# Kernel optimization log

Hardware: AMD Instinct MI355X
Metric: run time of the kernel (lower is better)

The kernel has to match this reference:

```python
import jax, jax.numpy as jnp
import numpy as np

N_FEAT = 1024
N_HEAD = 8
CONTEXT_SIZES = [21, 41]
HPS = N_HEAD // len(CONTEXT_SIZES)  # heads per scale = 4


def setup_inputs() -> dict:
    key = jax.random.key(0)
    ks = jax.random.split(key, 9)
    B, T, D = 4, 1024, N_FEAT
    s = 1.0 / np.sqrt(D)
    return {
        "query": jax.random.normal(ks[0], (B, T, D), dtype=jnp.float32),
        "key": jax.random.normal(ks[1], (B, T, D), dtype=jnp.float32),
        "value": jax.random.normal(ks[2], (B, T, D), dtype=jnp.float32),
        # weights stored [in, out] (torch Linear applies x @ W.T)
        "W_qv": jax.random.normal(ks[3], (D, 2 * D), dtype=jnp.float32) * s,
        "W2_0": jax.random.normal(ks[4], (D, HPS * CONTEXT_SIZES[0]), dtype=jnp.float32) * s,
        "W2_1": jax.random.normal(ks[5], (D, HPS * CONTEXT_SIZES[1]), dtype=jnp.float32) * s,
        "scale_weights": jnp.ones((len(CONTEXT_SIZES),), dtype=jnp.float32) / len(CONTEXT_SIZES),
        "W_out": jax.random.normal(ks[6], (D, D), dtype=jnp.float32) * s,
    }


def _sliding_window(v, c):
    # v: [B, T, D] -> [B, T, c, D], symmetric zero pad of (c-1)//2 each side
    B, T, D = v.shape
    half = (c - 1) // 2
    v_pad = jnp.pad(v, ((0, 0), (half, half), (0, 0)))
    idx = jnp.arange(T)[:, None] + jnp.arange(c)[None, :]  # [T, c]
    return v_pad[:, idx]  # [B, T, c, D]


def reference(query, key, value, W_qv, W2_0, W2_1, scale_weights, W_out):
    B, T, D = query.shape
    qv = query @ W_qv                      # [B, T, 2D]
    q, v = jnp.split(qv, 2, axis=-1)       # each [B, T, D]
    sw = jax.nn.softmax(scale_weights)     # [n_scales]
    head_dim = D // HPS
    x = jnp.zeros_like(query)
    for i, (c, W2) in enumerate(zip(CONTEXT_SIZES, [W2_0, W2_1])):
        # synthesized attention logits: [B, T, HPS, c]
        logits = (jax.nn.relu(q) @ W2).reshape(B, T, HPS, c)
        attn = jax.nn.softmax(logits, axis=-1)
        vw = _sliding_window(v, c).reshape(B, T, c, HPS, head_dim)
        out = jnp.einsum('bthc,btchd->bthd', attn, vw).reshape(B, T, D)
        x = x + sw[i] * out
    return x @ W_out
```

## Files before the change

kernel.cpp:

```cpp
#include <hip/hip_runtime.h>
#include <hip/hip_bf16.h>
#include <math.h>

#define BB 4
#define TT 1024
#define DD 1024
#define HPS 4
#define C0 21
#define C1 41
#define N0 (HPS * C0)
#define N1 (HPS * C1)
#define BT (BB * TT)
#define TB2 32
#define HALO 20
#define HB2 (TB2 + 2 * HALO)

typedef unsigned int uint;
typedef __bf16 bf16x8 __attribute__((ext_vector_type(8)));
typedef float f32x4 __attribute__((ext_vector_type(4)));

__device__ __forceinline__ ushort f2bf(float f) {
    union { float f; uint u; } v; v.f = f;
    uint u = v.u;
    uint r = (u + 0x7FFFu + ((u >> 16) & 1u)) >> 16;
    return (ushort)r;
}
__device__ __forceinline__ float bf2f(ushort s) {
    union { uint u; float f; } v; v.u = ((uint)s) << 16;
    return v.f;
}

#define RQ  4096
#define R1  (RQ + 2048)
#define R2  (R1 + 1024)
#define R3  (R2 + 96)
#define R4  (R3 + 192)

__device__ __forceinline__ void transpose_tile(
    const float* __restrict__ in, ushort* __restrict__ out,
    int K, int Nin, int nx, int ky, int tid, int hs, int roff)
{
    __shared__ float tile[32][33];
    const int tx = tid & 31;
    const int ty = tid >> 5;
    const int n0 = nx * 32;
    const int k0 = ky * 32;
    #pragma unroll
    for (int i = 0; i < 4; i++) {
        int k = k0 + ty + i * 8;
        int n = n0 + tx;
        float v = (k < K && n < Nin) ? in[(size_t)k * Nin + n] : 0.0f;
        tile[ty + i * 8][tx] = v;
    }
    __syncthreads();
    #pragma unroll
    for (int i = 0; i < 4; i++) {
        int n = n0 + ty + i * 8;
        int k = k0 + tx;
        if (n < Nin && k < K) {
            int row = (n / hs) * 64 + roff + (n % hs);
            out[(size_t)row * K + k] = f2bf(tile[tx][ty + i * 8]);
        }
    }
}

__global__ __launch_bounds__(256) void convert_all(
    const float* __restrict__ query, ushort* __restrict__ query_bf,
    const float* __restrict__ W_qv,  ushort* __restrict__ WqvT,
    const float* __restrict__ W_out, ushort* __restrict__ WoutT,
    const float* __restrict__ W2_0, const float* __restrict__ W2_1,
    ushort* __restrict__ W2Tph)
{
    const int blk = blockIdx.x;
    const int tid = threadIdx.x;
    if (blk < RQ) {
        int i = blk * 1024 + tid * 4;
        float4 v = *(const float4*)(query + i);
        ushort4 o;
        o.x = f2bf(v.x); o.y = f2bf(v.y); o.z = f2bf(v.z); o.w = f2bf(v.w);
        *(ushort4*)(query_bf + i) = o;
    } else if (blk < R1) {
        int idx = blk - RQ;
        transpose_tile(W_qv, WqvT, DD, 2 * DD, idx & 63, idx >> 6, tid, 2 * DD, 0);
    } else if (blk < R2) {
        int idx = blk - R1;
        transpose_tile(W_out, WoutT, DD, DD, idx & 31, idx >> 5, tid, DD, 0);
    } else if (blk < R3) {
        int idx = blk - R2;
        transpose_tile(W2_0, W2Tph, DD, N0, idx % 3, idx / 3, tid, C0, 0);
    } else {
        int idx = blk - R3;
        transpose_tile(W2_1, W2Tph, DD, N1, idx % 6, idx / 6, tid, C1, C0);
    }
}

__device__ __forceinline__ int xcd_chunk(int blk, int nblk) {
    return (blk & 7) * (nblk >> 3) + (blk >> 3);
}

template<int NT>
__global__ __launch_bounds__(512, 4) void gemm_mfma(
    const ushort* __restrict__ A, const ushort* __restrict__ Bt,
    int K, int klen,
    float* __restrict__ Cf, ushort* __restrict__ Cb, ushort* __restrict__ Cv,
    int mode, int ldc)
{
    constexpr int MT = 128;
    constexpr int MR = 4;
    constexpr int NR = NT / 64;
    __shared__ ushort As[2][MT * 64];
    __shared__ ushort Bs[2][NT * 64];

    const int tid = threadIdx.x;
    const int wv  = tid >> 6;
    const int ln  = tid & 63;

    const int ntile = gridDim.x * gridDim.y;
    const int tile  = xcd_chunk(blockIdx.y * gridDim.x + blockIdx.x, ntile);
    const int bx = tile % gridDim.x;
    const int by = tile / gridDim.x;
    const int row0 = by * MT;
    const int col0 = bx * NT;
    const int kbase = blockIdx.z * klen;

    const int wr = (wv >> 2) * 64;
    const int wc = (wv & 3) * (NT / 4);
    const int l15 = ln & 15;
    const int lq  = ln >> 4;

    f32x4 acc[MR][NR];
    #pragma unroll
    for (int i = 0; i < MR; i++)
        #pragma unroll
        for (int j = 0; j < NR; j++)
            acc[i][j] = (f32x4){0.f, 0.f, 0.f, 0.f};

    const int rsub = ln >> 3;
    const int cg   = (ln & 7) ^ rsub;
    const ushort* gA = A  + (size_t)(row0 + wv * 8 + rsub) * K + kbase + cg * 8;
    const ushort* gB = Bt + (size_t)(col0 + wv * 8 + rsub) * K + kbase + cg * 8;
    const int fx = l15 & 7;
    const int nt = klen / 64;

    auto STAGE = [&](int buf, int kk) {
        #pragma unroll
        for (int i = 0; i < 2; i++) {
            __builtin_amdgcn_global_load_lds(
                (const __attribute__((address_space(1))) void*)(gA + (size_t)i * 64 * K + kk),
                (__attribute__((address_space(3))) void*)(&As[buf][(i * 64 + wv * 8) * 64]),
                16, 0, 0);
        }
        #pragma unroll
        for (int i = 0; i < NT / 64; i++) {
            __builtin_amdgcn_global_load_lds(
                (const __attribute__((address_space(1))) void*)(gB + (size_t)i * 64 * K + kk),
                (__attribute__((address_space(3))) void*)(&Bs[buf][(i * 64 + wv * 8) * 64]),
                16, 0, 0);
        }
    };

    auto COMPUTE = [&](int buf) {
        #pragma unroll
        for (int s = 0; s < 2; s++) {
            const int ca = ((s * 4 + lq) ^ fx) * 8;
            bf16x8 af[MR], bfr[NR];
            #pragma unroll
            for (int mi = 0; mi < MR; mi++)
                af[mi] = *(const bf16x8*)&As[buf][(wr + mi * 16 + l15) * 64 + ca];
            #pragma unroll
            for (int ni = 0; ni < NR; ni++)
                bfr[ni] = *(const bf16x8*)&Bs[buf][(wc + ni * 16 + l15) * 64 + ca];
            #pragma unroll
            for (int mi = 0; mi < MR; mi++)
                #pragma unroll
                for (int ni = 0; ni < NR; ni++)
                    acc[mi][ni] = __builtin_amdgcn_mfma_f32_16x16x32_bf16(
                        af[mi], bfr[ni], acc[mi][ni], 0, 0, 0);
        }
    };

    int cur = 0;
    STAGE(0, 0);
    __syncthreads();
    for (int t = 0; t < nt; ++t) {
        const bool more = (t + 1 < nt);
        if (more) STAGE(cur ^ 1, (t + 1) * 64);
        COMPUTE(cur);
        if (more) __syncthreads();
        cur ^= 1;
    }

    #pragma unroll
    for (int mi = 0; mi < MR; mi++) {
        #pragma unroll
        for (int ni = 0; ni < NR; ni++) {
            #pragma unroll
            for (int r = 0; r < 4; r++) {
                int row = row0 + wr + mi * 16 + lq * 4 + r;
                int col = col0 + wc + ni * 16 + l15;
                float v = acc[mi][ni][r];
                if (mode == 0) {
                    Cf[(size_t)row * ldc + col] = v;
                } else {
                    if (col < DD) Cb[(size_t)row * DD + col] = f2bf(fmaxf(v, 0.0f));
                    else          Cv[(size_t)row * DD + (col - DD)] = f2bf(v);
                }
            }
        }
    }
}

#define LOFF_VS 0
#define LOFF_QS (LOFF_VS + HB2 * 256 * 2)
#define LOFF_WS (LOFF_QS + 2 * TB2 * 64 * 2)
#define LOFF_LS (LOFF_WS + 2 * 64 * 64 * 2)
#define LOFF_CW (LOFF_LS + TB2 * 65 * 4)
#define LDS_TOTAL (LOFF_CW + TB2 * 42 * 4)

__global__ __launch_bounds__(256) void attn_fused_kernel(
    const ushort* __restrict__ reluq,
    const ushort* __restrict__ W2Tph,
    const ushort* __restrict__ v,
    const float* __restrict__ scale_w,
    ushort* __restrict__ x)
{
    extern __shared__ __attribute__((aligned(16))) char smem[];
    ushort (*vs)[256] = (ushort (*)[256])(smem + LOFF_VS);
    ushort* qs = (ushort*)(smem + LOFF_QS);
    ushort* ws2 = (ushort*)(smem + LOFF_WS);
    float  (*Ls)[65] = (float (*)[65])(smem + LOFF_LS);
    float  (*cw)[42] = (float (*)[42])(smem + LOFF_CW);

    const int blk = blockIdx.x;
    const int h  = blk & 3;
    const int tt = (blk >> 2) & 31;
    const int b  = blk >> 7;
    const int t0 = tt * TB2;
    const int tid = threadIdx.x;
    const int bt0 = b * TT + t0;

    const ushort* vb = v + (size_t)b * TT * DD + h * 256;
    #pragma unroll
    for (int i = 0; i < 9; i++) {
        int c = i * 256 + tid;
        int r = c >> 5;
        int cir = c & 31;
        int t = t0 - HALO + r;
        uint4 val = make_uint4(0, 0, 0, 0);
        if (t >= 0 && t < TT)
            val = *(const uint4*)(vb + (size_t)t * DD + cir * 8);
        *(uint4*)(&vs[r][cir * 8]) = val;
    }

    const int wv = tid >> 6;
    const int ln = tid & 63;
    const int wr = (wv >> 1) * 16;
    const int wc = (wv & 1) * 32;
    const int l15 = ln & 15;
    const int lq  = ln >> 4;
    const int rsub = ln >> 3;
    const int cg   = (ln & 7) ^ rsub;
    const int fx = l15 & 7;

    const ushort* gA = reluq + (size_t)(bt0 + wv * 8 + rsub) * DD + cg * 8;
    const ushort* gB = W2Tph + ((size_t)h * 64 + wv * 16 + rsub) * DD + cg * 8;

    f32x4 acc[2];
    acc[0] = (f32x4){0.f, 0.f, 0.f, 0.f};
    acc[1] = (f32x4){0.f, 0.f, 0.f, 0.f};

    auto STAGEQ = [&](int buf, int kk) {
        __builtin_amdgcn_global_load_lds(
            (const __attribute__((address_space(1))) void*)(gA + kk),
            (__attribute__((address_space(3))) void*)(&qs[(size_t)buf * TB2 * 64 + (wv * 8) * 64]),
            16, 0, 0);
        #pragma unroll
        for (int i = 0; i < 2; i++) {
            __builtin_amdgcn_global_load_lds(
                (const __attribute__((address_space(1))) void*)(gB + (size_t)i * 8 * DD + kk),
                (__attribute__((address_space(3))) void*)(&ws2[(size_t)buf * 64 * 64 + (wv * 16 + i * 8) * 64]),
                16, 0, 0);
        }
    };
    auto COMPQ = [&](int buf) {
        #pragma unroll
        for (int s = 0; s < 2; s++) {
            const int ca = ((s * 4 + lq) ^ fx) * 8;
            bf16x8 a = *(const bf16x8*)&qs[(size_t)buf * TB2 * 64 + (wr + l15) * 64 + ca];
            #pragma unroll
            for (int ni = 0; ni < 2; ni++) {
                bf16x8 bb = *(const bf16x8*)&ws2[(size_t)buf * 64 * 64 + (wc + ni * 16 + l15) * 64 + ca];
                acc[ni] = __builtin_amdgcn_mfma_f32_16x16x32_bf16(a, bb, acc[ni], 0, 0, 0);
            }
        }
    };

    int cur = 0;
    STAGEQ(0, 0);
    __syncthreads();
    for (int t = 0; t < 16; ++t) {
        const bool more = (t + 1 < 16);
        if (more) STAGEQ(cur ^ 1, (t + 1) * 64);
        COMPQ(cur);
        if (more) __syncthreads();
        cur ^= 1;
    }
    #pragma unroll
    for (int ni = 0; ni < 2; ni++)
        #pragma unroll
        for (int r = 0; r < 4; r++)
            Ls[wr + lq * 4 + r][wc + ni * 16 + l15] = acc[ni][r];
    __syncthreads();

    if (tid < TB2) {
        float s0 = scale_w[0], s1 = scale_w[1];
        float mm = fmaxf(s0, s1);
        float e0 = __expf(s0 - mm), e1 = __expf(s1 - mm);
        float inv01 = 1.0f / (e0 + e1);
        float sw0 = e0 * inv01, sw1 = e1 * inv01;

        float w0[C0], w1[C1];
        {
            float m = -1e30f;
            #pragma unroll
            for (int j = 0; j < C0; j++) { w0[j] = Ls[tid][j]; m = fmaxf(m, w0[j]); }
            float s = 0.0f;
            #pragma unroll
            for (int j = 0; j < C0; j++) { w0[j] = __expf(w0[j] - m); s += w0[j]; }
            float inv = sw0 / s;
            #pragma unroll
            for (int j = 0; j < C0; j++) w0[j] *= inv;
        }
        {
            float m = -1e30f;
            #pragma unroll
            for (int j = 0; j < C1; j++) { w1[j] = Ls[tid][C0 + j]; m = fmaxf(m, w1[j]); }
            float s = 0.0f;
            #pragma unroll
            for (int j = 0; j < C1; j++) { w1[j] = __expf(w1[j] - m); s += w1[j]; }
            float inv = sw1 / s;
            #pragma unroll
            for (int j = 0; j < C1; j++) w1[j] *= inv;
        }
        #pragma unroll
        for (int o = 0; o < C1; o++) {
            float w = w1[o];
            if (o >= 10 && o <= 30) w += w0[o - 10];
            cw[tid][o] = w;
        }
    }
    __syncthreads();

    const int tq = tid >> 6;
    const int dg = tid & 63;
    const int d  = dg * 4;

    for (int tloc = 0; tloc < 8; tloc++) {
        const int tp = tq * 8 + tloc;
        f32x4 o4acc = {0.f, 0.f, 0.f, 0.f};
        #pragma unroll
        for (int o = 0; o < C1; o++) {
            float w = cw[tp][o];
            ushort4 vv = *(const ushort4*)(&vs[tp + o][d]);
            o4acc[0] = fmaf(w, bf2f(vv.x), o4acc[0]);
            o4acc[1] = fmaf(w, bf2f(vv.y), o4acc[1]);
            o4acc[2] = fmaf(w, bf2f(vv.z), o4acc[2]);
            o4acc[3] = fmaf(w, bf2f(vv.w), o4acc[3]);
        }
        const int bt = bt0 + tp;
        ushort4 o4;
        o4.x = f2bf(o4acc[0]); o4.y = f2bf(o4acc[1]);
        o4.z = f2bf(o4acc[2]); o4.w = f2bf(o4acc[3]);
        *(ushort4*)(x + (size_t)bt * DD + h * 256 + d) = o4;
    }
}

extern "C" void kernel_launch(void* const* d_in, const int* in_sizes, int n_in,
                              void* d_out, int out_size, void* d_ws, size_t ws_size,
                              hipStream_t stream)
{
    const float* query   = (const float*)d_in[0];
    const float* W_qv    = (const float*)d_in[3];
    const float* W2_0    = (const float*)d_in[4];
    const float* W2_1    = (const float*)d_in[5];
    const float* scale_w = (const float*)d_in[6];
    const float* W_out   = (const float*)d_in[7];
    float* out = (float*)d_out;

    char* ws = (char*)d_ws;
    ushort* W2Tph    = (ushort*)ws;                 ws += (size_t)4 * 64 * DD * 2;
    ushort* WoutT    = (ushort*)ws;                 ws += (size_t)DD * DD * 2;
    ushort* query_bf = (ushort*)ws;                 ws += (size_t)BT * DD * 2;
    ushort* WqvT     = (ushort*)ws;                 ws += (size_t)2 * DD * DD * 2;
    ushort* reluq    = (ushort*)ws;                 ws += (size_t)BT * DD * 2;
    ushort* vbuf     = (ushort*)ws;                 ws += (size_t)BT * DD * 2;
    ushort* xbuf     = (ushort*)ws;                 ws += (size_t)BT * DD * 2;

    convert_all<<<R4, 256, 0, stream>>>(query, query_bf, W_qv, WqvT,
                                        W_out, WoutT, W2_0, W2_1, W2Tph);

    {   dim3 grid(2 * DD / 128, BT / 128, 1);
        gemm_mfma<128><<<grid, 512, 0, stream>>>(query_bf, WqvT, DD, DD,
                                                 nullptr, reluq, vbuf, 2, 0); }
    attn_fused_kernel<<<512, 256, LDS_TOTAL, stream>>>(reluq, W2Tph, vbuf,
                                                       scale_w, xbuf);

    {   dim3 grid(DD / 64, BT / 128, 1);
        gemm_mfma<64><<<grid, 512, 0, stream>>>(xbuf, WoutT, DD, DD,
                                                out, nullptr, nullptr, 0, DD); }
}
```

Before: 168.1 us.

## Double attention block threads to 512 and raise output GEMM occupancy hint

The fused attention kernel now runs 8 waves per block instead of 4. Each wave computes one 16x16 MFMA tile of the logits, only the first four waves stage the query tile, and each thread aggregates 4 timesteps instead of 8 in the sliding-window sum. The output GEMM gets a launch-bounds hint of 6 waves per EU, and the unused split-K offset is removed. The aim is to hide latency in the attention stage through more parallel waves and to raise occupancy in the last GEMM, at the cost of more synchronisation per block and possible register pressure or spills.

After: 195.6 us. +16.4%, slower.

```diff
diff --git a/kernel.cpp b/kernel.cpp
--- a/kernel.cpp
+++ b/kernel.cpp
@@ -98,8 +98,8 @@
     return (blk & 7) * (nblk >> 3) + (blk >> 3);
 }
 
-template<int NT>
-__global__ __launch_bounds__(512, 4) void gemm_mfma(
+template<int NT, int MINW>
+__global__ __launch_bounds__(512, MINW) void gemm_mfma(
     const ushort* __restrict__ A, const ushort* __restrict__ Bt,
     int K, int klen,
     float* __restrict__ Cf, ushort* __restrict__ Cb, ushort* __restrict__ Cv,
@@ -121,7 +121,6 @@
     const int by = tile / gridDim.x;
     const int row0 = by * MT;
     const int col0 = bx * NT;
-    const int kbase = blockIdx.z * klen;
 
     const int wr = (wv >> 2) * 64;
     const int wc = (wv & 3) * (NT / 4);
@@ -137,8 +136,8 @@
 
     const int rsub = ln >> 3;
     const int cg   = (ln & 7) ^ rsub;
-    const ushort* gA = A  + (size_t)(row0 + wv * 8 + rsub) * K + kbase + cg * 8;
-    const ushort* gB = Bt + (size_t)(col0 + wv * 8 + rsub) * K + kbase + cg * 8;
+    const ushort* gA = A  + (size_t)(row0 + wv * 8 + rsub) * K + cg * 8;
+    const ushort* gB = Bt + (size_t)(col0 + wv * 8 + rsub) * K + cg * 8;
     const int fx = l15 & 7;
     const int nt = klen / 64;
 
@@ -217,7 +216,7 @@
 #define LOFF_CW (LOFF_LS + TB2 * 65 * 4)
 #define LDS_TOTAL (LOFF_CW + TB2 * 42 * 4)
 
-__global__ __launch_bounds__(256) void attn_fused_kernel(
+__global__ __launch_bounds__(512, 4) void attn_fused_kernel(
     const ushort* __restrict__ reluq,
     const ushort* __restrict__ W2Tph,
     const ushort* __restrict__ v,
@@ -241,57 +240,54 @@
 
     const ushort* vb = v + (size_t)b * TT * DD + h * 256;
     #pragma unroll
-    for (int i = 0; i < 9; i++) {
-        int c = i * 256 + tid;
-        int r = c >> 5;
-        int cir = c & 31;
-        int t = t0 - HALO + r;
-        uint4 val = make_uint4(0, 0, 0, 0);
-        if (t >= 0 && t < TT)
-            val = *(const uint4*)(vb + (size_t)t * DD + cir * 8);
-        *(uint4*)(&vs[r][cir * 8]) = val;
+    for (int i = 0; i < 5; i++) {
+        int c = i * 512 + tid;
+        if (c < HB2 * 32) {
+            int r = c >> 5;
+            int cir = c & 31;
+            int t = t0 - HALO + r;
+            uint4 val = make_uint4(0, 0, 0, 0);
+            if (t >= 0 && t < TT)
+                val = *(const uint4*)(vb + (size_t)t * DD + cir * 8);
+            *(uint4*)(&vs[r][cir * 8]) = val;
+        }
     }
 
     const int wv = tid >> 6;
     const int ln = tid & 63;
-    const int wr = (wv >> 1) * 16;
-    const int wc = (wv & 1) * 32;
+    const int wr = (wv >> 2) * 16;
+    const int wc = (wv & 3) * 16;
     const int l15 = ln & 15;
     const int lq  = ln >> 4;
     const int rsub = ln >> 3;
     const int cg   = (ln & 7) ^ rsub;
     const int fx = l15 & 7;
 
-    const ushort* gA = reluq + (size_t)(bt0 + wv * 8 + rsub) * DD + cg * 8;
-    const ushort* gB = W2Tph + ((size_t)h * 64 + wv * 16 + rsub) * DD + cg * 8;
-
-    f32x4 acc[2];
-    acc[0] = (f32x4){0.f, 0.f, 0.f, 0.f};
-    acc[1] = (f32x4){0.f, 0.f, 0.f, 0.f};
+    const int qrow = (wv & 3) * 8 + rsub;
+    const ushort* gA = reluq + (size_t)(bt0 + qrow) * DD + cg * 8;
+    const ushort* gB = W2Tph + ((size_t)h * 64 + wv * 8 + rsub) * DD + cg * 8;
+
+    f32x4 acc = (f32x4){0.f, 0.f, 0.f, 0.f};
 
     auto STAGEQ = [&](int buf, int kk) {
+        if (wv < 4) {
+            __builtin_amdgcn_global_load_lds(
+                (const __attribute__((address_space(1))) void*)(gA + kk),
+                (__attribute__((address_space(3))) void*)(&qs[(size_t)buf * TB2 * 64 + ((wv & 3) * 8) * 64]),
+                16, 0, 0);
+        }
         __builtin_amdgcn_global_load_lds(
-            (const __attribute__((address_space(1))) void*)(gA + kk),
-            (__attribute__((address_space(3))) void*)(&qs[(size_t)buf * TB2 * 64 + (wv * 8) * 64]),
+            (const __attribute__((address_space(1))) void*)(gB + kk),
+            (__attribute__((address_space(3))) void*)(&ws2[(size_t)buf * 64 * 64 + (wv * 8) * 64]),
             16, 0, 0);
-        #pragma unroll
-        for (int i = 0; i < 2; i++) {
-            __builtin_amdgcn_global_load_lds(
-                (const __attribute__((address_space(1))) void*)(gB + (size_t)i * 8 * DD + kk),
-                (__attribute__((address_space(3))) void*)(&ws2[(size_t)buf * 64 * 64 + (wv * 16 + i * 8) * 64]),
-                16, 0, 0);
-        }
     };
     auto COMPQ = [&](int buf) {
         #pragma unroll
         for (int s = 0; s < 2; s++) {
             const int ca = ((s * 4 + lq) ^ fx) * 8;
-            bf16x8 a = *(const bf16x8*)&qs[(size_t)buf * TB2 * 64 + (wr + l15) * 64 + ca];
-            #pragma unroll
-            for (int ni = 0; ni < 2; ni++) {
-                bf16x8 bb = *(const bf16x8*)&ws2[(size_t)buf * 64 * 64 + (wc + ni * 16 + l15) * 64 + ca];
-                acc[ni] = __builtin_amdgcn_mfma_f32_16x16x32_bf16(a, bb, acc[ni], 0, 0, 0);
-            }
+            bf16x8 a  = *(const bf16x8*)&qs[(size_t)buf * TB2 * 64 + (wr + l15) * 64 + ca];
+            bf16x8 bb = *(const bf16x8*)&ws2[(size_t)buf * 64 * 64 + (wc + l15) * 64 + ca];
+            acc = __builtin_amdgcn_mfma_f32_16x16x32_bf16(a, bb, acc, 0, 0, 0);
         }
     };
 
@@ -306,10 +302,8 @@
         cur ^= 1;
     }
     #pragma unroll
-    for (int ni = 0; ni < 2; ni++)
-        #pragma unroll
-        for (int r = 0; r < 4; r++)
-            Ls[wr + lq * 4 + r][wc + ni * 16 + l15] = acc[ni][r];
+    for (int r = 0; r < 4; r++)
+        Ls[wr + lq * 4 + r][wc + l15] = acc[r];
     __syncthreads();
 
     if (tid < TB2) {
@@ -355,8 +349,9 @@
     const int dg = tid & 63;
     const int d  = dg * 4;
 
-    for (int tloc = 0; tloc < 8; tloc++) {
-        const int tp = tq * 8 + tloc;
+    #pragma unroll
+    for (int tloc = 0; tloc < 4; tloc++) {
+        const int tp = tq * 4 + tloc;
         f32x4 o4acc = {0.f, 0.f, 0.f, 0.f};
         #pragma unroll
         for (int o = 0; o < C1; o++) {
@@ -400,12 +395,12 @@
                                         W_out, WoutT, W2_0, W2_1, W2Tph);
 
     {   dim3 grid(2 * DD / 128, BT / 128, 1);
-        gemm_mfma<128><<<grid, 512, 0, stream>>>(query_bf, WqvT, DD, DD,
-                                                 nullptr, reluq, vbuf, 2, 0); }
-    attn_fused_kernel<<<512, 256, LDS_TOTAL, stream>>>(reluq, W2Tph, vbuf,
+        gemm_mfma<128, 4><<<grid, 512, 0, stream>>>(query_bf, WqvT, DD, DD,
+                                                    nullptr, reluq, vbuf, 2, 0); }
+    attn_fused_kernel<<<512, 512, LDS_TOTAL, stream>>>(reluq, W2Tph, vbuf,
                                                        scale_w, xbuf);
 
     {   dim3 grid(DD / 64, BT / 128, 1);
-        gemm_mfma<64><<<grid, 512, 0, stream>>>(xbuf, WoutT, DD, DD,
-                                                out, nullptr, nullptr, 0, DD); }
-}
+        gemm_mfma<64, 6><<<grid, 512, 0, stream>>>(xbuf, WoutT, DD, DD,
+                                                   out, nullptr, nullptr, 0, DD); }
+}
```
